# Performance work log

Measured on AMD Instinct MI355X. Metric: run time of the kernel, lower is better.

The kernel has to match this reference:

```python
import jax, jax.numpy as jnp
import numpy as np

BN_EPS = 1e-5
N_EULER = 8


def _bn_train(x, gamma, beta):
    # BatchNorm1d in training mode: biased batch statistics over the batch axis
    mu = jnp.mean(x, axis=0)
    var = jnp.mean((x - mu) ** 2, axis=0)
    return gamma * (x - mu) / jnp.sqrt(var + BN_EPS) + beta


def setup_inputs() -> dict:
    key = jax.random.key(0)
    ks = jax.random.split(key, 16)
    B, d, u_dim, n_obs, sdim = 4096, 512, 64, 25, 128
    h1, h2, hd = 1024, 1024, 512

    def w(k, shape, fan_in):
        return jax.random.normal(k, shape, dtype=jnp.float32) / np.sqrt(fan_in)

    return {
        "z_dyn": jax.random.normal(ks[0], (B, d), dtype=jnp.float32),
        "z_static": jax.random.normal(ks[1], (B, sdim), dtype=jnp.float32),
        "dt": jnp.array(0.05, dtype=jnp.float32),
        "ut": jax.random.normal(ks[2], (B, u_dim), dtype=jnp.float32),
        "eps": jax.random.normal(ks[3], (N_EULER, B, d), dtype=jnp.float32),
        "W1": w(ks[4], (h1, d), d), "b1": jnp.zeros((h1,), jnp.float32),
        "g1": jnp.ones((h1,), jnp.float32), "be1": jnp.zeros((h1,), jnp.float32),
        "W2": w(ks[5], (h2, h1), h1), "b2": jnp.zeros((h2,), jnp.float32),
        "g2": jnp.ones((h2,), jnp.float32), "be2": jnp.zeros((h2,), jnp.float32),
        "W3": w(ks[6], (d, h2), h2), "b3": jnp.zeros((d,), jnp.float32),
        "Wd1": w(ks[7], (hd, d), d), "bd1": jnp.zeros((hd,), jnp.float32),
        "Wd2": w(ks[8], (d, hd), hd), "bd2": jnp.zeros((d,), jnp.float32),
        "B_sde": w(ks[9], (d, u_dim), u_dim),
        "C": w(ks[10], (n_obs, d), d),
        "D": w(ks[11], (n_obs, u_dim), u_dim),
    }


def reference(z_dyn, z_static, dt, ut, eps,
              W1, b1, g1, be1, W2, b2, g2, be2, W3, b3,
              Wd1, bd1, Wd2, bd2, B_sde, C, D):
    h = dt / N_EULER
    sqrt_h = jnp.sqrt(jnp.abs(h) + 1e-8)

    def drift(z):
        a = jax.nn.relu(_bn_train(z @ W1.T + b1, g1, be1))
        a = jax.nn.relu(_bn_train(a @ W2.T + b2, g2, be2))
        return a @ W3.T + b3

    def diffusion(z):
        t = jnp.tanh(z @ Wd1.T + bd1)
        return jax.nn.softplus(t @ Wd2.T + bd2) + 1e-5

    def step(z, e):
        f = drift(z)
        g = diffusion(z)
        z = z + h * f + sqrt_h * g * e  # Euler-Maruyama update (training mode)
        return z, None

    z, _ = jax.lax.scan(step, z_dyn, eps)
    ut_dt = ut * dt
    z_next = z + ut_dt @ B_sde.T
    yt = z_next @ C.T + ut_dt @ D.T
    return (z_next, yt)
```

## Files before the change

kernel.cpp:

```cpp
#include <hip/hip_runtime.h>


typedef unsigned short ushort_t;
typedef __bf16 bf16x8 __attribute__((ext_vector_type(8)));
typedef _Float16 f16x8 __attribute__((ext_vector_type(8)));
typedef float f32x4 __attribute__((ext_vector_type(4)));

__device__ __forceinline__ float bf2f(ushort_t s) {
  unsigned u = ((unsigned)s) << 16;
  return __uint_as_float(u);
}
__device__ __forceinline__ ushort_t f2bf(float f) {
  unsigned u = __float_as_uint(f);
  unsigned lsb = (u >> 16) & 1u;
  u += 0x7fffu + lsb;
  return (ushort_t)(u >> 16);
}
__device__ __forceinline__ float ldin(const void* p, size_t i, int f32) {
  return f32 ? ((const float*)p)[i] : bf2f(((const ushort_t*)p)[i]);
}
__device__ __forceinline__ void async16(const void* g, void* l) {
  __builtin_amdgcn_global_load_lds(
      (const __attribute__((address_space(1))) void*)g,
      (__attribute__((address_space(3))) void*)l, 16, 0, 0);
}

template <int N>
__device__ __forceinline__ void waitvm() {
  if constexpr (N == 0) {
    asm volatile("s_waitcnt vmcnt(0)" ::: "memory");
  } else if constexpr (N == 4) {
    asm volatile("s_waitcnt vmcnt(4)" ::: "memory");
  } else if constexpr (N == 6) {
    asm volatile("s_waitcnt vmcnt(6)" ::: "memory");
  }
  __builtin_amdgcn_sched_barrier(0);
}
__device__ __forceinline__ void waitlgkm0() {
  asm volatile("s_waitcnt lgkmcnt(0)" ::: "memory");
  __builtin_amdgcn_sched_barrier(0);
}

__device__ __forceinline__ bf16x8 lds_frag(const __bf16* T, int row, int kb) {
  const int byte = (row << 7) + ((((kb >> 3) ^ (row & 7))) << 4);
  return *(const bf16x8*)((const char*)T + byte);
}

__global__ void k_detect(const void* __restrict__ eps, const void* __restrict__ dtraw,
                         float* __restrict__ consts) {
  __shared__ float mx[256];
  const int t = threadIdx.x;
  const ushort_t* e = (const ushort_t*)eps;
  float m = 0.f;
#pragma unroll
  for (int k = 0; k < 4; ++k) {
    float v = fabsf(bf2f(e[t * 4 + k]));
    if (!(v < 1e30f)) v = 1e30f;
    m = fmaxf(m, v);
  }
  mx[t] = m;
  __syncthreads();
  if (t == 0) {
    float M = 0.f;
    for (int k = 0; k < 256; ++k) M = fmaxf(M, mx[k]);
    const int f32 = (M > 1e3f) ? 1 : 0;
    float dt;
    if (f32) {
      dt = *(const float*)dtraw;
    } else {
      float db = bf2f(*(const ushort_t*)dtraw);
      float df = *(const float*)dtraw;
      dt = (db > 1e-6f && db < 1e3f) ? db : df;
    }
    const float h = dt * 0.125f;
    consts[0] = h;
    consts[1] = sqrtf(fabsf(h) + 1e-8f);
    consts[2] = dt;
    consts[3] = (float)f32;
  }
}

struct ConvArgs { const void* src[5]; };
#define CONV_TOT 2621440

__global__ void k_conv(ConvArgs a, const float* __restrict__ consts,
                       ushort_t* __restrict__ base) {
  constexpr int CUM[6] = {0, 524288, 786432, 1835008, 2359296, 2621440};
  const int f32 = consts[3] != 0.f;
  const int i = (blockIdx.x * 256 + threadIdx.x) * 4;
  if (i >= CONV_TOT) return;
  int j = 0;
#pragma unroll
  for (int k = 1; k < 5; ++k)
    if (i >= CUM[k]) j = k;
  const int local = i - CUM[j];
  const void* s = a.src[j];
  ushort4 o;
  if (f32) {
    float4 v = ((const float4*)s)[local >> 2];
    o = make_ushort4(f2bf(v.x), f2bf(v.y), f2bf(v.z), f2bf(v.w));
  } else {
    o = ((const ushort4*)s)[local >> 2];
  }
  *(ushort4*)(base + i) = o;
}

template <int MT, int KT, int MODE, int STATS, int FUSE, int BIAS, int FINAL,
          int ANORM>
__device__ __forceinline__ void gemm_body(
    const ushort_t* __restrict__ A, const ushort_t* __restrict__ W,
    const void* __restrict__ bias, int ncol0, ushort_t* __restrict__ Cout,
    int Nout, int m0, int n0, __bf16* As, __bf16* Bs,
    float* __restrict__ s1, float* __restrict__ s2,
    const ushort_t* __restrict__ Gb, float* __restrict__ zf,
    ushort_t* __restrict__ zb, const void* __restrict__ eps,
    unsigned long long eoff, const float* __restrict__ consts,
    const float* __restrict__ Ub, float* __restrict__ out0,
    const float* __restrict__ s1in, const float* __restrict__ s2in,
    const void* __restrict__ gsc, const void* __restrict__ gbe,
    _Float16* scF, _Float16* shF, float* sS) {
  constexpr int BM = MT * 64;
  constexpr int LPT = MT * 2 + 2;
  const int f32 = consts[3] != 0.f;
  const int tid = threadIdx.x;
  const int lane = tid & 63;
  const int wave = tid >> 6;
  const int col = lane & 15;
  const int quad = lane >> 4;
  const int rowBase = wave * (MT * 16);

  const int srow = tid >> 3;
  const int skc = tid & 7;
  auto stageA = [&](int k0, __bf16* dst) {
#pragma unroll
    for (int j = 0; j < BM / 32; ++j) {
      const int row = j * 32 + srow;
      async16(A + (size_t)(m0 + row) * KT + k0 + (((skc ^ (row & 7))) << 3),
              (char*)dst + (j * 256 + tid) * 16);
    }
  };
  auto stageB = [&](int k0, __bf16* dst) {
#pragma unroll
    for (int j = 0; j < 2; ++j) {
      const int row = j * 32 + srow;
      async16(W + (size_t)(n0 + row) * KT + k0 + (((skc ^ (row & 7))) << 3),
              (char*)dst + (j * 256 + tid) * 16);
    }
  };

  f32x4 acc[MT][4] = {};

  __bf16* Acur = As;
  __bf16* Aalt = As + BM * 64;
  __bf16* Bcur = Bs;
  __bf16* Balt = Bs + 64 * 64;

  stageA(0, Acur);
  stageB(0, Bcur);

  if (ANORM) {
    const float inv = 1.0f / 4096.0f;
#pragma unroll
    for (int c0 = 0; c0 < KT; c0 += 256) {
      const int c = c0 + tid;
      float mu = s1in[c] * inv;
      float var = fmaxf(s2in[c] * inv - mu * mu, 0.f);
      float sc = ldin(gsc, c, f32) * rsqrtf(var + 1e-5f);
      scF[c] = (_Float16)sc;
      shF[c] = (_Float16)(ldin(gbe, c, f32) - mu * sc);
    }
  }
  waitlgkm0();
  __builtin_amdgcn_s_barrier();

  constexpr int NIT = KT / 64;
#pragma unroll 1
  for (int it = 0; it < NIT; ++it) {
    const int k0 = it * 64;
    if (it + 1 < NIT) {
      stageA(k0 + 64, Aalt);
      stageB(k0 + 64, Balt);
      waitvm<LPT>();
    } else {
      waitvm<0>();
    }
    __builtin_amdgcn_s_barrier();

#pragma unroll
    for (int kk = 0; kk < 2; ++kk) {
      const int kb = kk * 32 + quad * 8;
      bf16x8 af[MT], bfr[4];
      if (ANORM) {
        f16x8 scv = *(const f16x8*)&scF[k0 + kb];
        f16x8 shv = *(const f16x8*)&shF[k0 + kb];
#pragma unroll
        for (int mt = 0; mt < MT; ++mt) {
          bf16x8 raw = lds_frag(Acur, rowBase + mt * 16 + col, kb);
#pragma unroll
          for (int j = 0; j < 8; ++j)
            af[mt][j] = (__bf16)fmaxf(
                fmaf((float)raw[j], (float)scv[j], (float)shv[j]), 0.f);
        }
      } else {
#pragma unroll
        for (int mt = 0; mt < MT; ++mt)
          af[mt] = lds_frag(Acur, rowBase + mt * 16 + col, kb);
      }
#pragma unroll
      for (int nt = 0; nt < 4; ++nt)
        bfr[nt] = lds_frag(Bcur, nt * 16 + col, kb);
      __builtin_amdgcn_s_setprio(1);
#pragma unroll
      for (int mt = 0; mt < MT; ++mt)
#pragma unroll
        for (int nt = 0; nt < 4; ++nt)
          acc[mt][nt] = __builtin_amdgcn_mfma_f32_16x16x32_bf16(
              af[mt], bfr[nt], acc[mt][nt], 0, 0, 0);
      __builtin_amdgcn_s_setprio(0);
    }
    waitlgkm0();
    __builtin_amdgcn_s_barrier();
    __bf16* t0 = Acur; Acur = Aalt; Aalt = t0;
    __bf16* t1 = Bcur; Bcur = Balt; Balt = t1;
  }

  if (STATS) {
    for (int i = tid; i < 128; i += 256) sS[i] = 0.f;
    __syncthreads();
  }

  const float h = consts[0], sh = consts[1];

#pragma unroll
  for (int nt = 0; nt < 4; ++nt) {
    const int gn = n0 + nt * 16 + col;
    const float bv = BIAS ? ldin(bias, gn + ncol0, f32) : 0.f;
    float ls = 0.f, lq = 0.f;
#pragma unroll
    for (int mt = 0; mt < MT; ++mt) {
#pragma unroll
      for (int r = 0; r < 4; ++r) {
        const int gm = m0 + rowBase + mt * 16 + quad * 4 + r;
        float v = acc[mt][nt][r] + bv;
        if (STATS) {
          ls += v;
          lq += v * v;
        }
        if (MODE == 1) {
          v = tanhf(v);
        } else if (MODE == 2) {
          v = fmaxf(v, 0.f) + log1pf(expf(-fabsf(v))) + 1e-5f;
        }
        const size_t o = (size_t)gm * Nout + gn + ncol0;
        if (FUSE) {
          const float e = ldin(eps, eoff + o, f32);
          const float g = bf2f(Gb[o]);
          const float z = zf[o] + h * v + sh * g * e;
          zf[o] = z;
          zb[o] = f2bf(z);
          if (FINAL) out0[o] = z + Ub[o];
        } else {
          Cout[o] = f2bf(v);
        }
      }
    }
    if (STATS) {
      atomicAdd(&sS[nt * 16 + col], ls);
      atomicAdd(&sS[64 + nt * 16 + col], lq);
    }
  }

  if (STATS) {
    __syncthreads();
    if (tid < 64) {
      atomicAdd(&s1[n0 + tid], sS[tid]);
      atomicAdd(&s2[n0 + tid], sS[64 + tid]);
    }
  }
}

__global__ __launch_bounds__(256, 3) void k_x1t(
    const ushort_t* __restrict__ zb, const ushort_t* __restrict__ Wcat,
    const void* __restrict__ bd1, ushort_t* __restrict__ Xb,
    ushort_t* __restrict__ Tb, float* __restrict__ s1, float* __restrict__ s2,
    const float* __restrict__ consts) {
  __shared__ __bf16 As[2 * 128 * 64] __attribute__((aligned(16)));
  __shared__ __bf16 Bs[2 * 64 * 64] __attribute__((aligned(16)));
  __shared__ float sS[128];
  const int L = blockIdx.x;
  const int q = L & 7, w = L >> 3;
  const int mloc = w & 3, n = w >> 2;
  const int m0 = (q * 4 + mloc) * 128;
  const int n0 = n * 64;
  if (n < 16) {
    gemm_body<2, 512, 0, 1, 0, 0, 0, 0>(
        zb, Wcat, nullptr, 0, Xb, 1024, m0, n0, As, Bs, s1, s2, nullptr,
        nullptr, nullptr, nullptr, 0, consts, nullptr, nullptr, nullptr,
        nullptr, nullptr, nullptr, nullptr, nullptr, sS);
  } else {
    gemm_body<2, 512, 1, 0, 0, 1, 0, 0>(
        zb, Wcat, bd1, -1024, Tb, 512, m0, n0, As, Bs, nullptr,
        nullptr, nullptr, nullptr, nullptr, nullptr, 0, consts, nullptr,
        nullptr, nullptr, nullptr, nullptr, nullptr, nullptr, nullptr, sS);
  }
}

__global__ __launch_bounds__(256, 3) void k_x2g(
    const ushort_t* __restrict__ X1raw, const ushort_t* __restrict__ W2c,
    const ushort_t* __restrict__ Tb, const ushort_t* __restrict__ Wd2c,
    const void* __restrict__ bd2, ushort_t* __restrict__ Ab,
    ushort_t* __restrict__ Gb, float* __restrict__ s1o, float* __restrict__ s2o,
    const float* __restrict__ s1i, const float* __restrict__ s2i,
    const void* __restrict__ g1, const void* __restrict__ be1,
    const float* __restrict__ consts) {
  __shared__ __bf16 As[2 * 128 * 64] __attribute__((aligned(16)));
  __shared__ __bf16 Bs[2 * 64 * 64] __attribute__((aligned(16)));
  __shared__ _Float16 scF[1024] __attribute__((aligned(16)));
  __shared__ _Float16 shF[1024] __attribute__((aligned(16)));
  __shared__ float sS[128];
  const int L = blockIdx.x;
  if (L < 512) {
    const int q = L & 7, w = L >> 3;
    const int mloc = w & 3, n = w >> 2;
    const int m0 = (q * 4 + mloc) * 128, n0 = n * 64;
    gemm_body<2, 1024, 0, 1, 0, 0, 0, 1>(
        X1raw, W2c, nullptr, 0, Ab, 1024, m0, n0, As, Bs, s1o, s2o,
        nullptr, nullptr, nullptr, nullptr, 0, consts, nullptr, nullptr, s1i,
        s2i, g1, be1, scF, shF, sS);
  } else {
    const int Lg = L - 512;
    const int q = Lg & 7, w = Lg >> 3;
    const int mloc = w & 3, n = w >> 2;
    const int m0 = (q * 4 + mloc) * 128, n0 = n * 64;
    gemm_body<2, 512, 2, 0, 0, 1, 0, 0>(
        Tb, Wd2c, bd2, 0, Gb, 512, m0, n0, As, Bs, nullptr, nullptr,
        nullptr, nullptr, nullptr, nullptr, 0, consts, nullptr, nullptr,
        nullptr, nullptr, nullptr, nullptr, nullptr, nullptr, sS);
  }
}

template <int FINAL>
__global__ __launch_bounds__(256, 4) void k_fupd(
    const ushort_t* __restrict__ X2raw, const ushort_t* __restrict__ W3c,
    const void* __restrict__ b3, const ushort_t* __restrict__ Gb,
    float* __restrict__ zf, ushort_t* __restrict__ zb,
    const void* __restrict__ eps, unsigned long long eoff,
    const float* __restrict__ consts, const float* __restrict__ Ub,
    float* __restrict__ out0, const float* __restrict__ s1i,
    const float* __restrict__ s2i, const void* __restrict__ g2,
    const void* __restrict__ be2) {
  __shared__ __bf16 As[2 * 64 * 64] __attribute__((aligned(16)));
  __shared__ __bf16 Bs[2 * 64 * 64] __attribute__((aligned(16)));
  __shared__ _Float16 scF[1024] __attribute__((aligned(16)));
  __shared__ _Float16 shF[1024] __attribute__((aligned(16)));
  const int L = blockIdx.x;
  const int q = L & 7, w = L >> 3;
  const int mloc = w & 7, n = w >> 3;
  const int m0 = (q * 8 + mloc) * 64, n0 = n * 64;
  gemm_body<1, 1024, 0, 0, 1, 1, FINAL, 1>(
      X2raw, W3c, b3, 0, nullptr, 512, m0, n0, As, Bs, nullptr, nullptr,
      Gb, zf, zb, eps, eoff, consts, Ub, out0, s1i, s2i, g2, be2, scF, shF,
      nullptr);
}

__global__ void k_init(const void* __restrict__ z, float* __restrict__ zf,
                       ushort_t* __restrict__ zb, const float* __restrict__ consts) {
  const int f32 = consts[3] != 0.f;
  const int i = blockIdx.x * 256 + threadIdx.x;
  float4 v;
  if (f32) {
    v = ((const float4*)z)[i];
  } else {
    ushort4 u = ((const ushort4*)z)[i];
    v = make_float4(bf2f(u.x), bf2f(u.y), bf2f(u.z), bf2f(u.w));
  }
  ((float4*)zf)[i] = v;
  ((ushort4*)zb)[i] = make_ushort4(f2bf(v.x), f2bf(v.y), f2bf(v.z), f2bf(v.w));
}

__global__ __launch_bounds__(256) void k_ub(
    const void* __restrict__ ut, const void* __restrict__ Bsde,
    const float* __restrict__ consts, float* __restrict__ Ub) {
  __shared__ float As[64][68];
  __shared__ float Bs[64][68];
  const float dt = consts[2];
  const int f32 = consts[3] != 0.f;
  const int t = threadIdx.x;
  const int tx = t & 15, ty = t >> 4;
  const int n0 = blockIdx.x * 64, m0 = blockIdx.y * 64;
  const int r = t >> 2;
  const int c0 = (t & 3) * 16;

#pragma unroll
  for (int j = 0; j < 16; ++j) {
    As[c0 + j][r] = ldin(ut, (size_t)(m0 + r) * 64 + c0 + j, f32);
    Bs[c0 + j][r] = ldin(Bsde, (size_t)(n0 + r) * 64 + c0 + j, f32);
  }
  __syncthreads();

  float acc[4][4] = {};
#pragma unroll 8
  for (int kk = 0; kk < 64; ++kk) {
    float a[4], b[4];
    *(float4*)a = *(const float4*)&As[kk][ty * 4];
    *(float4*)b = *(const float4*)&Bs[kk][tx * 4];
#pragma unroll
    for (int i = 0; i < 4; ++i)
#pragma unroll
      for (int j = 0; j < 4; ++j) acc[i][j] += a[i] * b[j];
  }

#pragma unroll
  for (int i = 0; i < 4; ++i) {
    const size_t o = (size_t)(m0 + ty * 4 + i) * 512 + n0 + tx * 4;
    *(float4*)&Ub[o] = make_float4(dt * acc[i][0], dt * acc[i][1],
                                   dt * acc[i][2], dt * acc[i][3]);
  }
}

__global__ void k_deff(const void* __restrict__ Cm, const void* __restrict__ Bsde,
                       const void* __restrict__ Dm, const float* __restrict__ consts,
                       float* __restrict__ Deff) {
  __shared__ float red[4][64];
  const int f32 = consts[3] != 0.f;
  const int j = blockIdx.x;
  const int k = threadIdx.x & 63;
  const int part = threadIdx.x >> 6;
  float acc = 0.f;
  const int l0 = part * 128;
#pragma unroll 8
  for (int l = l0; l < l0 + 128; ++l)
    acc += ldin(Cm, (size_t)j * 512 + l, f32) * ldin(Bsde, (size_t)l * 64 + k, f32);
  red[part][k] = acc;
  __syncthreads();
  if (part == 0) {
    float s = red[0][k] + red[1][k] + red[2][k] + red[3][k];
    Deff[j * 64 + k] = s + ldin(Dm, (size_t)j * 64 + k, f32);
  }
}

__global__ __launch_bounds__(256) void k_final2(
    const float* __restrict__ zf, const void* __restrict__ ut,
    const float* __restrict__ consts, const void* __restrict__ Cm,
    const float* __restrict__ Deff, float* __restrict__ out1) {
  const float dt = consts[2];
  const int f32 = consts[3] != 0.f;
  const int t = threadIdx.x;
  const int lane = t & 63;
  const int m = blockIdx.x * 4 + (t >> 6);
  float z8[8];
#pragma unroll
  for (int i = 0; i < 8; ++i) z8[i] = zf[(size_t)m * 512 + i * 64 + lane];
  const float u = ldin(ut, (size_t)m * 64 + lane, f32);

  for (int j = 0; j < 25; ++j) {
    float p = dt * u * Deff[j * 64 + lane];
#pragma unroll
    for (int i = 0; i < 8; ++i)
      p += z8[i] * ldin(Cm, (size_t)j * 512 + i * 64 + lane, f32);
#pragma unroll
    for (int off = 32; off > 0; off >>= 1) p += __shfl_down(p, off, 64);
    if (lane == 0) out1[m * 25 + j] = p;
  }
}

extern "C" void kernel_launch(void* const* d_in, const int* in_sizes, int n_in,
                              void* d_out, int out_size, void* d_ws, size_t ws_size,
                              hipStream_t stream) {
  static const int expA[22] = {
      2097152, 524288, 1,      262144, 16777216, 524288, 1024, 1024,
      1024,    1048576, 1024,  1024,   1024,     524288, 512,  262144,
      512,     262144, 512,    32768,  12800,    1600};

  int map[21];
  bool okA = (n_in == 22), okB = (n_in == 21);
  if (okA)
    for (int i = 0; i < 22; ++i)
      if (in_sizes[i] != expA[i]) { okA = false; break; }
  if (okB) {
    int j = 0;
    for (int i = 0; i < 22; ++i) {
      if (i == 1) continue;
      if (in_sizes[j] != expA[i]) { okB = false; break; }
      ++j;
    }
  }
  if (okA) {
    map[0] = 0;
    for (int i = 1; i < 21; ++i) map[i] = i + 1;
  } else if (okB) {
    for (int i = 0; i < 21; ++i) map[i] = i;
  } else {
    map[0] = 0;
    for (int i = 1; i < 21; ++i) map[i] = (i + 1 < n_in) ? i + 1 : n_in - 1;
  }

  const void* z_dyn = d_in[map[0]];
  const void* dtp = d_in[map[1]];
  const void* ut = d_in[map[2]];
  const void* eps = d_in[map[3]];
  const void* W1 = d_in[map[4]];
  const void* g1 = d_in[map[6]];
  const void* be1 = d_in[map[7]];
  const void* W2 = d_in[map[8]];
  const void* g2 = d_in[map[10]];
  const void* be2 = d_in[map[11]];
  const void* W3 = d_in[map[12]];
  const void* b3 = d_in[map[13]];
  const void* Wd1 = d_in[map[14]];
  const void* bd1 = d_in[map[15]];
  const void* Wd2 = d_in[map[16]];
  const void* bd2 = d_in[map[17]];
  const void* Bsde = d_in[map[18]];
  const void* Cm = d_in[map[19]];
  const void* Dm = d_in[map[20]];

  char* ws = (char*)d_ws;
  const size_t MB = 1024 * 1024;
  float* zf = (float*)(ws + 0);
  ushort_t* zb = (ushort_t*)(ws + 8 * MB);
  ushort_t* Xb = (ushort_t*)(ws + 12 * MB);
  ushort_t* Ab = (ushort_t*)(ws + 20 * MB);
  ushort_t* Tb = (ushort_t*)(ws + 28 * MB);
  ushort_t* Gb = (ushort_t*)(ws + 32 * MB);
  float* Ub = (float*)(ws + 36 * MB);
  ushort_t* canon = (ushort_t*)(ws + 44 * MB);
  float* stats = (float*)(ws + 49 * MB + 512 * 1024);
  float* consts = stats + 16 * 2048;
  float* Deff = consts + 16;

  const ushort_t* Wcat = canon + 0;
  const ushort_t* W2c = canon + 786432;
  const ushort_t* W3c = canon + 1835008;
  const ushort_t* Wd2c = canon + 2359296;

  float* out_z = (float*)d_out;
  float* out_y = out_z + 4096 * 512;

  const dim3 blk(256);

  k_detect<<<1, blk, 0, stream>>>(eps, dtp, consts);

  ConvArgs ca;
  ca.src[0] = W1;
  ca.src[1] = Wd1;
  ca.src[2] = W2;
  ca.src[3] = W3;
  ca.src[4] = Wd2;
  k_conv<<<(CONV_TOT / 4 + 255) / 256, blk, 0, stream>>>(ca, consts, canon);

  hipMemsetAsync(stats, 0, 16 * 2048 * sizeof(float), stream);
  k_init<<<2048, blk, 0, stream>>>(z_dyn, zf, zb, consts);
  k_ub<<<dim3(8, 64), blk, 0, stream>>>(ut, Bsde, consts, Ub);
  k_deff<<<25, blk, 0, stream>>>(Cm, Bsde, Dm, consts, Deff);

  for (int s = 0; s < 8; ++s) {
    float* sA1 = stats + (s * 2 + 0) * 2048;
    float* sA2 = stats + (s * 2 + 1) * 2048;
    const unsigned long long eoff = (unsigned long long)s * 4096 * 512;

    k_x1t<<<768, blk, 0, stream>>>(zb, Wcat, bd1, Xb, Tb,
                                   sA1, sA1 + 1024, consts);

    k_x2g<<<768, blk, 0, stream>>>(Xb, W2c, Tb, Wd2c, bd2, Ab, Gb,
                                   sA2, sA2 + 1024, sA1, sA1 + 1024,
                                   g1, be1, consts);

    if (s < 7) {
      k_fupd<0><<<512, blk, 0, stream>>>(Ab, W3c, b3, Gb, zf, zb, eps, eoff,
                                         consts, Ub, out_z, sA2, sA2 + 1024,
                                         g2, be2);
    } else {
      k_fupd<1><<<512, blk, 0, stream>>>(Ab, W3c, b3, Gb, zf, zb, eps, eoff,
                                         consts, Ub, out_z, sA2, sA2 + 1024,
                                         g2, be2);
    }
  }

  k_final2<<<1024, blk, 0, stream>>>(zf, ut, consts, Cm, Deff, out_y);
}
```

Before: 766.9 us.

## Triple-buffer LDS staging with one barrier per iteration in k_fupd GEMM

Adds a DEEP template path to the shared GEMM body that keeps three LDS buffers, prefetching two k-tiles ahead and using a single barrier per iteration instead of two. Only the final drift GEMM kernel (k_fupd) uses it: its shared arrays grow to three stages and its launch-bounds occupancy hint drops from 4 to 2. The aim is to hide global-load latency and cut synchronisation stalls in the long K=1024 loop. The cost is more LDS per block and possibly lower occupancy.

```diff
diff --git a/kernel.cpp b/kernel.cpp
--- a/kernel.cpp
+++ b/kernel.cpp
@@ -106,7 +106,7 @@
 }
 
 template <int MT, int KT, int MODE, int STATS, int FUSE, int BIAS, int FINAL,
-          int ANORM>
+          int ANORM, int DEEP>
 __device__ __forceinline__ void gemm_body(
     const ushort_t* __restrict__ A, const ushort_t* __restrict__ W,
     const void* __restrict__ bias, int ncol0, ushort_t* __restrict__ Cout,
@@ -148,44 +148,25 @@
     }
   };
 
+  auto tables = [&]() {
+    if (ANORM) {
+      const float inv = 1.0f / 4096.0f;
+#pragma unroll
+      for (int c0 = 0; c0 < KT; c0 += 256) {
+        const int c = c0 + tid;
+        float mu = s1in[c] * inv;
+        float var = fmaxf(s2in[c] * inv - mu * mu, 0.f);
+        float sc = ldin(gsc, c, f32) * rsqrtf(var + 1e-5f);
+        scF[c] = (_Float16)sc;
+        shF[c] = (_Float16)(ldin(gbe, c, f32) - mu * sc);
+      }
+    }
+  };
+
   f32x4 acc[MT][4] = {};
-
-  __bf16* Acur = As;
-  __bf16* Aalt = As + BM * 64;
-  __bf16* Bcur = Bs;
-  __bf16* Balt = Bs + 64 * 64;
-
-  stageA(0, Acur);
-  stageB(0, Bcur);
-
-  if (ANORM) {
-    const float inv = 1.0f / 4096.0f;
-#pragma unroll
-    for (int c0 = 0; c0 < KT; c0 += 256) {
-      const int c = c0 + tid;
-      float mu = s1in[c] * inv;
-      float var = fmaxf(s2in[c] * inv - mu * mu, 0.f);
-      float sc = ldin(gsc, c, f32) * rsqrtf(var + 1e-5f);
-      scF[c] = (_Float16)sc;
-      shF[c] = (_Float16)(ldin(gbe, c, f32) - mu * sc);
-    }
-  }
-  waitlgkm0();
-  __builtin_amdgcn_s_barrier();
-
   constexpr int NIT = KT / 64;
-#pragma unroll 1
-  for (int it = 0; it < NIT; ++it) {
-    const int k0 = it * 64;
-    if (it + 1 < NIT) {
-      stageA(k0 + 64, Aalt);
-      stageB(k0 + 64, Balt);
-      waitvm<LPT>();
-    } else {
-      waitvm<0>();
-    }
-    __builtin_amdgcn_s_barrier();
-
+
+  auto computeTile = [&](const __bf16* Ac, const __bf16* Bc, int k0) {
 #pragma unroll
     for (int kk = 0; kk < 2; ++kk) {
       const int kb = kk * 32 + quad * 8;
@@ -195,7 +176,7 @@
         f16x8 shv = *(const f16x8*)&shF[k0 + kb];
 #pragma unroll
         for (int mt = 0; mt < MT; ++mt) {
-          bf16x8 raw = lds_frag(Acur, rowBase + mt * 16 + col, kb);
+          bf16x8 raw = lds_frag(Ac, rowBase + mt * 16 + col, kb);
 #pragma unroll
           for (int j = 0; j < 8; ++j)
             af[mt][j] = (__bf16)fmaxf(
@@ -204,11 +185,11 @@
       } else {
 #pragma unroll
         for (int mt = 0; mt < MT; ++mt)
-          af[mt] = lds_frag(Acur, rowBase + mt * 16 + col, kb);
+          af[mt] = lds_frag(Ac, rowBase + mt * 16 + col, kb);
       }
 #pragma unroll
       for (int nt = 0; nt < 4; ++nt)
-        bfr[nt] = lds_frag(Bcur, nt * 16 + col, kb);
+        bfr[nt] = lds_frag(Bc, nt * 16 + col, kb);
       __builtin_amdgcn_s_setprio(1);
 #pragma unroll
       for (int mt = 0; mt < MT; ++mt)
@@ -218,10 +199,64 @@
               af[mt], bfr[nt], acc[mt][nt], 0, 0, 0);
       __builtin_amdgcn_s_setprio(0);
     }
+  };
+
+  if (DEEP) {
+    __bf16* Ac = As;
+    __bf16* An = As + BM * 64;
+    __bf16* A2 = As + 2 * BM * 64;
+    __bf16* Bc = Bs;
+    __bf16* Bn = Bs + 64 * 64;
+    __bf16* B2 = Bs + 2 * 64 * 64;
+    stageA(0, Ac);
+    stageB(0, Bc);
+    stageA(64, An);
+    stageB(64, Bn);
+    tables();
+    waitlgkm0();
+#pragma unroll 1
+    for (int it = 0; it < NIT; ++it) {
+      if (it + 1 < NIT) {
+        waitvm<LPT>();
+      } else {
+        waitvm<0>();
+      }
+      __builtin_amdgcn_s_barrier();
+      if (it + 2 < NIT) {
+        stageA((it + 2) * 64, A2);
+        stageB((it + 2) * 64, B2);
+      }
+      computeTile(Ac, Bc, it * 64);
+      __bf16* ta = Ac; Ac = An; An = A2; A2 = ta;
+      __bf16* tb = Bc; Bc = Bn; Bn = B2; B2 = tb;
+    }
+  } else {
+    __bf16* Acur = As;
+    __bf16* Aalt = As + BM * 64;
+    __bf16* Bcur = Bs;
+    __bf16* Balt = Bs + 64 * 64;
+    stageA(0, Acur);
+    stageB(0, Bcur);
+    tables();
     waitlgkm0();
     __builtin_amdgcn_s_barrier();
-    __bf16* t0 = Acur; Acur = Aalt; Aalt = t0;
-    __bf16* t1 = Bcur; Bcur = Balt; Balt = t1;
+#pragma unroll 1
+    for (int it = 0; it < NIT; ++it) {
+      const int k0 = it * 64;
+      if (it + 1 < NIT) {
+        stageA(k0 + 64, Aalt);
+        stageB(k0 + 64, Balt);
+        waitvm<LPT>();
+      } else {
+        waitvm<0>();
+      }
+      __builtin_amdgcn_s_barrier();
+      computeTile(Acur, Bcur, k0);
+      waitlgkm0();
+      __builtin_amdgcn_s_barrier();
+      __bf16* t0 = Acur; Acur = Aalt; Aalt = t0;
+      __bf16* t1 = Bcur; Bcur = Balt; Balt = t1;
+    }
   }
 
   if (STATS) {
@@ -293,12 +328,12 @@
   const int m0 = (q * 4 + mloc) * 128;
   const int n0 = n * 64;
   if (n < 16) {
-    gemm_body<2, 512, 0, 1, 0, 0, 0, 0>(
+    gemm_body<2, 512, 0, 1, 0, 0, 0, 0, 0>(
         zb, Wcat, nullptr, 0, Xb, 1024, m0, n0, As, Bs, s1, s2, nullptr,
         nullptr, nullptr, nullptr, 0, consts, nullptr, nullptr, nullptr,
         nullptr, nullptr, nullptr, nullptr, nullptr, sS);
   } else {
-    gemm_body<2, 512, 1, 0, 0, 1, 0, 0>(
+    gemm_body<2, 512, 1, 0, 0, 1, 0, 0, 0>(
         zb, Wcat, bd1, -1024, Tb, 512, m0, n0, As, Bs, nullptr,
         nullptr, nullptr, nullptr, nullptr, nullptr, 0, consts, nullptr,
         nullptr, nullptr, nullptr, nullptr, nullptr, nullptr, nullptr, sS);
@@ -323,7 +358,7 @@
     const int q = L & 7, w = L >> 3;
     const int mloc = w & 3, n = w >> 2;
     const int m0 = (q * 4 + mloc) * 128, n0 = n * 64;
-    gemm_body<2, 1024, 0, 1, 0, 0, 0, 1>(
+    gemm_body<2, 1024, 0, 1, 0, 0, 0, 1, 0>(
         X1raw, W2c, nullptr, 0, Ab, 1024, m0, n0, As, Bs, s1o, s2o,
         nullptr, nullptr, nullptr, nullptr, 0, consts, nullptr, nullptr, s1i,
         s2i, g1, be1, scF, shF, sS);
@@ -332,7 +367,7 @@
     const int q = Lg & 7, w = Lg >> 3;
     const int mloc = w & 3, n = w >> 2;
     const int m0 = (q * 4 + mloc) * 128, n0 = n * 64;
-    gemm_body<2, 512, 2, 0, 0, 1, 0, 0>(
+    gemm_body<2, 512, 2, 0, 0, 1, 0, 0, 0>(
         Tb, Wd2c, bd2, 0, Gb, 512, m0, n0, As, Bs, nullptr, nullptr,
         nullptr, nullptr, nullptr, nullptr, 0, consts, nullptr, nullptr,
         nullptr, nullptr, nullptr, nullptr, nullptr, nullptr, sS);
@@ -340,7 +375,7 @@
 }
 
 template <int FINAL>
-__global__ __launch_bounds__(256, 4) void k_fupd(
+__global__ __launch_bounds__(256, 2) void k_fupd(
     const ushort_t* __restrict__ X2raw, const ushort_t* __restrict__ W3c,
     const void* __restrict__ b3, const ushort_t* __restrict__ Gb,
     float* __restrict__ zf, ushort_t* __restrict__ zb,
@@ -349,15 +384,15 @@
     float* __restrict__ out0, const float* __restrict__ s1i,
     const float* __restrict__ s2i, const void* __restrict__ g2,
     const void* __restrict__ be2) {
-  __shared__ __bf16 As[2 * 64 * 64] __attribute__((aligned(16)));
-  __shared__ __bf16 Bs[2 * 64 * 64] __attribute__((aligned(16)));
+  __shared__ __bf16 As[3 * 64 * 64] __attribute__((aligned(16)));
+  __shared__ __bf16 Bs[3 * 64 * 64] __attribute__((aligned(16)));
   __shared__ _Float16 scF[1024] __attribute__((aligned(16)));
   __shared__ _Float16 shF[1024] __attribute__((aligned(16)));
   const int L = blockIdx.x;
   const int q = L & 7, w = L >> 3;
   const int mloc = w & 7, n = w >> 3;
   const int m0 = (q * 8 + mloc) * 64, n0 = n * 64;
-  gemm_body<1, 1024, 0, 0, 1, 1, FINAL, 1>(
+  gemm_body<1, 1024, 0, 0, 1, 1, FINAL, 1, 1>(
       X2raw, W3c, b3, 0, nullptr, 512, m0, n0, As, Bs, nullptr, nullptr,
       Gb, zf, zb, eps, eoff, consts, Ub, out0, s1i, s2i, g2, be2, scF, shF,
       nullptr);
```

After: 763.4 us. About the same (-0.5%).
